# Kernel optimization log

Measured on AMD Instinct MI355X. Metric: run time of the kernel, lower is better.

Reference implementation:

```python
import jax, jax.numpy as jnp
import numpy as np

B, DIM, H, W = 2, 48, 256, 256
HEADS = 8
CHEAD = DIM // HEADS
HID = int(DIM * 2)


def _conv2d(x, w, stride=1, pad=0, dil=1, groups=1):
    return jax.lax.conv_general_dilated(
        x, w, (stride, stride), [(pad, pad), (pad, pad)],
        rhs_dilation=(dil, dil), feature_group_count=groups,
        dimension_numbers=('NCHW', 'OIHW', 'NCHW'))


def _ln(x, w, b):
    # WithBias LayerNorm over the channel axis (to_3d makes channels the last dim)
    mu = jnp.mean(x, axis=1, keepdims=True)
    var = jnp.mean((x - mu) ** 2, axis=1, keepdims=True)
    return (x - mu) / jnp.sqrt(var + 1e-5) * w[None, :, None, None] + b[None, :, None, None]


def _gelu(x):
    return jax.nn.gelu(x, approximate=False)


def setup_inputs() -> dict:
    key = jax.random.key(0)
    ks = iter(jax.random.split(key, 40))
    nrm = lambda *s: jax.random.normal(next(ks), s, dtype=jnp.float32) * 0.02
    d = dict(
        x=jax.random.normal(next(ks), (B, DIM, H, W), dtype=jnp.float32),
        ln1_w=jnp.ones(DIM), ln1_b=jnp.zeros(DIM),
        qkv_w=nrm(3 * DIM, DIM),            # 1x1x1 Conv3d == channel linear
        qkv_dw_w=nrm(3 * DIM, 1, 3, 3),     # center depth slice of 3x3x3 depthwise (depth=1 input)
        proj_w=nrm(DIM, DIM),
        fc_w=nrm(9, 3 * HEADS), fc_b=jnp.zeros(9),
        dep_w=nrm(DIM, 9, 3, 3), dep_b=jnp.zeros(DIM),  # groups = dim//heads
        l2q_w=nrm(DIM, DIM), l2q_b=jnp.zeros(DIM),
        temperature=jnp.ones(HEADS),
        ln2_w=jnp.ones(DIM), ln2_b=jnp.zeros(DIM),
        pin_w=nrm(3 * HID, DIM),
        dw1_w=nrm(HID, 1, 3, 3), dw2_w=nrm(HID, 1, 3, 3), dw3_w=nrm(HID, 1, 3, 3),
        pout_w=nrm(DIM, HID),
    )
    for i in range(3):
        d[f'cv_w{i}'] = nrm(DIM, DIM, 3, 3)
        d[f'cv_b{i}'] = jnp.zeros(DIM)
        d[f'cln_w{i}'] = jnp.ones(DIM)
        d[f'cln_b{i}'] = jnp.zeros(DIM)
    return d


def _forward(x, ln1_w, ln1_b, qkv_w, qkv_dw_w, proj_w, fc_w, fc_b, dep_w, dep_b,
             l2q_w, l2q_b, temperature, ln2_w, ln2_b, pin_w, dw1_w, dw2_w, dw3_w,
             pout_w, cv_w0, cv_b0, cln_w0, cln_b0, cv_w1, cv_b1, cln_w1, cln_b1,
             cv_w2, cv_b2, cln_w2, cln_b2):
    b, c, h, w = x.shape
    heads = temperature.shape[0]
    chead = c // heads

    # ---- Conv2DTransformer branch -> pooled descriptor x_d [b, c]
    t = x
    for cw, cb, lw, lb in ((cv_w0, cv_b0, cln_w0, cln_b0),
                           (cv_w1, cv_b1, cln_w1, cln_b1),
                           (cv_w2, cv_b2, cln_w2, cln_b2)):
        t = _conv2d(t, cw, stride=2, pad=1) + cb[None, :, None, None]
        t = jax.nn.relu(_ln(t, lw, lb))
        t = jax.lax.reduce_window(t, -jnp.inf, jax.lax.max, (1, 1, 2, 2), (1, 1, 2, 2), 'VALID')
    x_d = _gelu(jnp.mean(t, axis=(2, 3)))  # [b, c]

    # ---- Attention
    xn = _ln(x, ln1_w, ln1_b)
    qkv = jnp.einsum('oc,bchw->bohw', qkv_w, xn)
    qkv = _conv2d(qkv, qkv_dw_w, pad=1, groups=3 * c)  # depthwise, [b,3c,h,w]

    # conv-attention path: raw-memory reshape exactly as torch .reshape
    f_all = qkv.reshape(b, h * w, 3 * heads, chead).transpose(0, 2, 1, 3)  # [b,3H,hw,chead]
    f_all = jnp.einsum('oi,bipc->bopc', fc_w, f_all) + fc_b[None, :, None, None]  # [b,9,hw,chead]
    f_conv = f_all.transpose(0, 3, 1, 2).reshape(b, 9 * chead, h, w)
    out_conv = _conv2d(f_conv, dep_w, pad=1, groups=chead) + dep_b[None, :, None, None]

    # outer-product bias from pooled descriptor
    q0 = (x_d @ l2q_w.T + l2q_b).reshape(b, heads, chead)
    q0m = q0[:, :, :, None] * q0[:, :, None, :]  # [b,head,chead,chead]

    q, k, v = jnp.split(qkv, 3, axis=1)
    rs = lambda t_: t_.reshape(b, heads, chead, h * w)
    q, k, v = rs(q), rs(k), rs(v)
    nz = lambda t_: t_ / jnp.maximum(jnp.linalg.norm(t_, axis=-1, keepdims=True), 1e-12)
    q, k = nz(q), nz(k)

    attn = jnp.einsum('bhcx,bhdx->bhcd', q, k) * temperature[None, :, None, None]
    attn = jax.nn.softmax(attn * q0m, axis=-1)
    out = jnp.einsum('bhcd,bhdx->bhcx', attn, v).reshape(b, c, h, w)
    out = jnp.einsum('oc,bchw->bohw', proj_w, out) + out_conv

    x = x + out

    # ---- FeedForward (3-branch dilated depthwise)
    xn2 = _ln(x, ln2_w, ln2_b)
    y = jnp.einsum('oc,bchw->bohw', pin_w, xn2)  # [b,3*hid,h,w]
    hid = y.shape[1] // 3
    y1, y2, y3 = jnp.split(y, 3, axis=1)
    y1 = _conv2d(y1, dw1_w, pad=1, groups=hid)
    y2 = _conv2d(y2, dw2_w, pad=2, dil=2, groups=hid)
    y3 = _conv2d(y3, dw3_w, pad=3, dil=3, groups=hid)
    y = _gelu(y1) * y2 * y3
    return x + jnp.einsum('oc,bchw->bohw', pout_w, y)


def reference(x, ln1_w, ln1_b, qkv_w, qkv_dw_w, proj_w, fc_w, fc_b, dep_w, dep_b,
              l2q_w, l2q_b, temperature, ln2_w, ln2_b, pin_w, dw1_w, dw2_w, dw3_w,
              pout_w, cv_w0, cv_b0, cln_w0, cln_b0, cv_w1, cv_b1, cln_w1, cln_b1,
              cv_w2, cv_b2, cln_w2, cln_b2):
    return _forward(x, ln1_w, ln1_b, qkv_w, qkv_dw_w, proj_w, fc_w, fc_b, dep_w, dep_b,
                    l2q_w, l2q_b, temperature, ln2_w, ln2_b, pin_w, dw1_w, dw2_w, dw3_w,
                    pout_w, cv_w0, cv_b0, cln_w0, cln_b0, cv_w1, cv_b1, cln_w1, cln_b1,
                    cv_w2, cv_b2, cln_w2, cln_b2)
```

## Files before the change

### kernel.cpp

```cpp
#include <hip/hip_runtime.h>

constexpr int NB = 2;
constexpr int NC = 48;
constexpr int NH = 256;
constexpr int NW = 256;
constexpr int NP = NH * NW;
constexpr int NHEADS = 8;
constexpr int NCHD = 6;
constexpr int NHID = 96;
constexpr int GSEG = 64;

typedef unsigned short bf16_t;
typedef __attribute__((ext_vector_type(8))) short bf16x8;
typedef __attribute__((ext_vector_type(4))) float f32x4;

__device__ __forceinline__ float bf2f(bf16_t u) {
  union { unsigned int i; float f; } c; c.i = ((unsigned int)u) << 16; return c.f;
}
__device__ __forceinline__ bf16_t f2bf(float f) {
  union { float f; unsigned int i; } c; c.f = f;
  unsigned int r = (c.i + 0x7FFFu + ((c.i >> 16) & 1u)) >> 16;
  return (bf16_t)r;
}
__device__ __forceinline__ void unpack2(unsigned int u, float& a, float& b) {
  union { unsigned int i; float f; } c0, c1;
  c0.i = u << 16; c1.i = u & 0xffff0000u;
  a = c0.f; b = c1.f;
}

__device__ __forceinline__ float gelu_f(float v) {
  float u = v * (0.79788456f + 0.0356774081f * v * v);
  u = fminf(fmaxf(u, -9.f), 9.f);
  float e = __expf(-2.f * u);
  float th = (1.f - e) / (1.f + e);
  return 0.5f * v * (1.f + th);
}

#define STENCIL_ROW(LROW, D, WVAL0, WVAL1, WVAL2, ACC)                        \
  {                                                                            \
    const float* lp = &lds[(LROW) * 272 + quad * 4];                           \
    float4 va = *(const float4*)lp;                                            \
    float4 vb = *(const float4*)(lp + 4);                                      \
    float4 vc = *(const float4*)(lp + 8);                                      \
    float v[12] = {va.x, va.y, va.z, va.w, vb.x, vb.y, vb.z, vb.w,             \
                   vc.x, vc.y, vc.z, vc.w};                                    \
    _Pragma("unroll") for (int jj = 0; jj < 4; ++jj) {                         \
      ACC[jj] = fmaf(v[jj - (D) + 4], WVAL0, ACC[jj]);                         \
      ACC[jj] = fmaf(v[jj + 4], WVAL1, ACC[jj]);                               \
      ACC[jj] = fmaf(v[jj + (D) + 4], WVAL2, ACC[jj]);                         \
    }                                                                          \
  }

__global__ void k_prepw(const float* __restrict__ cvw0, bf16_t* __restrict__ WC) {
  int i = blockIdx.x * blockDim.x + threadIdx.x;
  if (i >= 9 * 3 * 2 * 512) return;
  int j = i & 7, lane = (i >> 3) & 63;
  int fi = i >> 9;
  int s = fi & 1;
  int tot = fi >> 1;
  int ot = tot % 3, t = tot / 3;
  int o = ot * 16 + (lane & 15);
  int k = s * 32 + ((lane >> 4) << 3) + j;
  float v = (k < 48) ? cvw0[(size_t)(o * 48 + k) * 9 + t] : 0.f;
  WC[i] = f2bf(v);
}

__global__ __launch_bounds__(512) void k_conv1_mfma(const float* __restrict__ in,
                                                    const bf16_t* __restrict__ WC,
                                                    const float* __restrict__ bias,
                                                    float* __restrict__ out) {
  __shared__ bf16_t xs[17 * 17 * 72];
  __shared__ float red[4 * 3 * 64 * 4];
  int blk = blockIdx.x;
  int tx = blk & 15;
  int t0 = blk >> 4;
  int ty = t0 & 15, b = t0 >> 4;
  int oy0 = ty * 8, ox0 = tx * 8;
  int iy0 = oy0 * 2 - 1, ix0 = ox0 * 2 - 1;
  const float* inb = in + (size_t)b * NC * NP;
  for (int i = threadIdx.x; i < 17 * 17 * 48; i += 512) {
    int cc = i % 17;
    int t2 = i / 17;
    int rr = t2 % 17;
    int ic = t2 / 17;
    float v = 0.f;
    int iy = iy0 + rr, ix = ix0 + cc;
    if ((unsigned)iy < 256u && (unsigned)ix < 256u)
      v = inb[((size_t)ic << 16) + (iy << 8) + ix];
    xs[(rr * 17 + cc) * 72 + ic] = f2bf(v);
  }
  for (int i = threadIdx.x; i < 289 * 16; i += 512) {
    int rcc = i >> 4, icz = i & 15;
    xs[rcc * 72 + 48 + icz] = 0;
  }
  __syncthreads();
  int wid = threadIdx.x >> 6, lane = threadIdx.x & 63;
  int pt = wid & 3, s = wid >> 2;
  int l15 = lane & 15, kl = lane >> 4;
  int px = pt * 16 + l15;
  int oy = px >> 3, ox = px & 7;
  int base = ((oy * 2) * 17 + ox * 2) * 72 + s * 32 + kl * 8;
  f32x4 acc[3] = {{0.f, 0.f, 0.f, 0.f}, {0.f, 0.f, 0.f, 0.f}, {0.f, 0.f, 0.f, 0.f}};
  #pragma unroll
  for (int t = 0; t < 9; ++t) {
    int dy = t / 3, dx = t % 3;
    bf16x8 bf = *(const bf16x8*)&xs[base + dy * (17 * 72) + dx * 72];
    #pragma unroll
    for (int ot = 0; ot < 3; ++ot) {
      bf16x8 af = *(const bf16x8*)(WC + (size_t)((t * 3 + ot) * 2 + s) * 512 + lane * 8);
      acc[ot] = __builtin_amdgcn_mfma_f32_16x16x32_bf16(af, bf, acc[ot], 0, 0, 0);
    }
  }
  if (s == 1) {
    #pragma unroll
    for (int ot = 0; ot < 3; ++ot)
      #pragma unroll
      for (int j = 0; j < 4; ++j)
        red[((pt * 3 + ot) * 64 + lane) * 4 + j] = acc[ot][j];
  }
  __syncthreads();
  if (s == 0) {
    float* ob = out + (size_t)b * NC * 16384;
    #pragma unroll
    for (int ot = 0; ot < 3; ++ot) {
      #pragma unroll
      for (int j = 0; j < 4; ++j) {
        int o = ot * 16 + kl * 4 + j;
        float r = acc[ot][j] + red[((pt * 3 + ot) * 64 + lane) * 4 + j] + bias[o];
        ob[((size_t)o * 128 + oy0 + oy) * 128 + ox0 + ox] = r;
      }
    }
  }
}

__global__ __launch_bounds__(512) void k_conv_s2_tile(const float* __restrict__ in,
                                                      const float* __restrict__ w,
                                                      const float* __restrict__ bias,
                                                      float* __restrict__ out,
                                                      int IH, int IW, int OH, int OW) {
  __shared__ float lds[16 * 442];
  int tilesX = OW >> 3;
  int tilesY = OH >> 3;
  int blk = blockIdx.x;
  int tx = blk % tilesX;
  int t = blk / tilesX;
  int ty = t % tilesY;
  int b = t / tilesY;
  int oy0 = ty * 8, ox0 = tx * 8;
  int iy0 = oy0 * 2 - 1, ix0 = ox0 * 2 - 1;
  const float* inb = in + (size_t)b * NC * IH * IW;

  int lane = threadIdx.x & 63;
  int oy = lane >> 3, ox = lane & 7;
  int ocb = __builtin_amdgcn_readfirstlane((threadIdx.x >> 6) * 6);
  float acc[6];
  #pragma unroll
  for (int j = 0; j < 6; ++j) acc[j] = bias[ocb + j];
  int rbase = oy * 52;

  for (int chunk = 0; chunk < 3; ++chunk) {
    int icb = chunk * 16;
    for (int i = threadIdx.x; i < 16 * 17 * 17; i += 512) {
      int cc = i % 17;
      int t2 = i / 17;
      int rr = t2 % 17;
      int ic = t2 / 17;
      float v = 0.f;
      int iy = iy0 + rr, ix = ix0 + cc;
      if ((unsigned)iy < (unsigned)IH && (unsigned)ix < (unsigned)IW)
        v = inb[((size_t)(icb + ic) * IH + iy) * IW + ix];
      lds[ic * 442 + rr * 26 + ((cc & 1) ? 13 + (cc >> 1) : (cc >> 1))] = v;
    }
    __syncthreads();

    for (int ic16 = 0; ic16 < 16; ++ic16) {
      const float* base = lds + ic16 * 442 + rbase;
      float e0[3], e1[3], ov[3];
      #pragma unroll
      for (int ky = 0; ky < 3; ++ky) {
        const float* rowp = base + ky * 26;
        e0[ky] = rowp[ox];
        e1[ky] = rowp[ox + 1];
        ov[ky] = rowp[13 + ox];
      }
      const float* wpc = w + (size_t)(ocb * 48 + icb + ic16) * 9;
      #pragma unroll
      for (int j = 0; j < 6; ++j) {
        const float* wp = wpc + (size_t)j * 48 * 9;
        float a = acc[j];
        #pragma unroll
        for (int ky = 0; ky < 3; ++ky) {
          a = fmaf(wp[ky * 3 + 0], e0[ky], a);
          a = fmaf(wp[ky * 3 + 1], ov[ky], a);
          a = fmaf(wp[ky * 3 + 2], e1[ky], a);
        }
        acc[j] = a;
      }
    }
    __syncthreads();
  }

  float* ob = out + (size_t)b * NC * OH * OW;
  #pragma unroll
  for (int j = 0; j < 6; ++j)
    ob[((size_t)(ocb + j) * OH + oy0 + oy) * OW + ox0 + ox] = acc[j];
}

__global__ void k_lnpool(const float* __restrict__ in, const float* __restrict__ lw,
                         const float* __restrict__ lb, float* __restrict__ out,
                         int IH, int IW) {
  int OH = IH >> 1, OW = IW >> 1;
  int idx = blockIdx.x * blockDim.x + threadIdx.x;
  int total = NB * OH * OW;
  if (idx >= total) return;
  int ox = idx % OW;
  int t = idx / OW;
  int oy = t % OH;
  int b = t / OH;
  const float* inb = in + (size_t)b * NC * IH * IW;
  float mu[4], rs[4];
  #pragma unroll
  for (int q = 0; q < 4; ++q) {
    int iy = oy * 2 + (q >> 1), ix = ox * 2 + (q & 1);
    float s = 0.f, ss = 0.f;
    for (int c = 0; c < NC; ++c) {
      float v = inb[((size_t)c * IH + iy) * IW + ix];
      s += v; ss += v * v;
    }
    float m = s * (1.f / NC);
    mu[q] = m;
    rs[q] = rsqrtf(fmaxf(ss * (1.f / NC) - m * m, 0.f) + 1e-5f);
  }
  for (int c = 0; c < NC; ++c) {
    float best = 0.f;
    float wv = lw[c], bv = lb[c];
    #pragma unroll
    for (int q = 0; q < 4; ++q) {
      int iy = oy * 2 + (q >> 1), ix = ox * 2 + (q & 1);
      float v = inb[((size_t)c * IH + iy) * IW + ix];
      v = (v - mu[q]) * rs[q] * wv + bv;
      best = fmaxf(best, fmaxf(v, 0.f));
    }
    out[((size_t)(b * NC + c) * OH + oy) * OW + ox] = best;
  }
}

__global__ void k_head(const float* __restrict__ p3, const float* __restrict__ l2qw,
                       const float* __restrict__ l2qb, float* __restrict__ q0m) {
  __shared__ float xd[NC], q0[NC];
  int b = blockIdx.x, t = threadIdx.x;
  if (t < NC) {
    float s = 0.f;
    for (int i = 0; i < 16; ++i) s += p3[(b * NC + t) * 16 + i];
    xd[t] = gelu_f(s * (1.f / 16.f));
  }
  __syncthreads();
  if (t < NC) {
    float a = l2qb[t];
    for (int c = 0; c < NC; ++c) a += xd[c] * l2qw[t * NC + c];
    q0[t] = a;
  }
  __syncthreads();
  if (t < NHEADS * NCHD * NCHD) {
    int h = t / 36, r = t % 36, c = r / 6, d = r % 6;
    q0m[b * 288 + t] = q0[h * 6 + c] * q0[h * 6 + d];
  }
}

__global__ void k_prep(const float* __restrict__ qkvw, const float* __restrict__ ln1w,
                       const float* __restrict__ ln1b, const float* __restrict__ pinw,
                       const float* __restrict__ ln2w, const float* __restrict__ ln2b,
                       const float* __restrict__ poutw, const float* __restrict__ projw,
                       float* __restrict__ SB, bf16_t* __restrict__ WA1,
                       bf16_t* __restrict__ WA2, bf16_t* __restrict__ WP,
                       bf16_t* __restrict__ WJ) {
  int t = blockIdx.x * blockDim.x + threadIdx.x;
  int stride = gridDim.x * blockDim.x;
  if (t < 144) {
    float s = 0.f, bb = 0.f;
    for (int c = 0; c < 48; ++c) {
      float w = qkvw[t * 48 + c];
      s = fmaf(w, ln1w[c], s); bb = fmaf(w, ln1b[c], bb);
    }
    SB[t] = s; SB[144 + t] = bb;
  } else if (t < 144 + 288) {
    int o = t - 144;
    float s = 0.f, bb = 0.f;
    for (int c = 0; c < 48; ++c) {
      float w = pinw[o * 48 + c];
      s = fmaf(w, ln2w[c], s); bb = fmaf(w, ln2b[c], bb);
    }
    SB[288 + o] = s; SB[576 + o] = bb;
  }
  for (int i = t; i < 9 * 1024; i += stride) {
    int j = i & 7, lane = (i >> 3) & 63, s = (i >> 9) & 1, ot = i >> 10;
    int o = ot * 16 + (lane & 15);
    int k = s * 32 + ((lane >> 4) << 3) + j;
    float v = (k < 48) ? qkvw[o * 48 + k] * ln1w[k] : 0.f;
    WA1[i] = f2bf(v);
  }
  for (int i = t; i < 18 * 1024; i += stride) {
    int j = i & 7, lane = (i >> 3) & 63, s = (i >> 9) & 1, ot = i >> 10;
    int o = ot * 16 + (lane & 15);
    int k = s * 32 + ((lane >> 4) << 3) + j;
    float v = (k < 48) ? pinw[o * 48 + k] * ln2w[k] : 0.f;
    WA2[i] = f2bf(v);
  }
  for (int i = t; i < 9 * 512; i += stride) {
    int j = i & 7, lane = (i >> 3) & 63;
    int fi = i >> 9;
    int s = fi % 3, ot = fi / 3;
    int o = ot * 16 + (lane & 15);
    int k = s * 32 + ((lane >> 4) << 3) + j;
    WP[i] = f2bf(poutw[o * 96 + k]);
  }
  for (int i = t; i < 6 * 512; i += stride) {
    int j = i & 7, lane = (i >> 3) & 63;
    int fi = i >> 9;
    int s = fi & 1, ot = fi >> 1;
    int o = ot * 16 + (lane & 15);
    int k = s * 32 + ((lane >> 4) << 3) + j;
    float v = (k < 48) ? projw[o * 48 + k] : 0.f;
    WJ[i] = f2bf(v);
  }
}

__global__ __launch_bounds__(256) void k_chmix_mfma(const float* __restrict__ x,
                                                    const bf16_t* __restrict__ WA,
                                                    const float* __restrict__ S,
                                                    const float* __restrict__ Bc,
                                                    bf16_t* __restrict__ out,
                                                    int nout) {
  __shared__ bf16_t xT[64 * 72];
  __shared__ float smu[64], srstd[64];
  int blk = blockIdx.x;
  int pxt = blk & 1023;
  int b = blk >> 10;
  int pbase = pxt * 64;
  const float* xb = x + (size_t)b * NC * NP + pbase;
  int p4 = threadIdx.x & 15, k0 = threadIdx.x >> 4;
  #pragma unroll
  for (int it = 0; it < 3; ++it) {
    int k = k0 + it * 16;
    float4 v = *(const float4*)(xb + (size_t)k * NP + p4 * 4);
    xT[(p4 * 4 + 0) * 72 + k] = f2bf(v.x);
    xT[(p4 * 4 + 1) * 72 + k] = f2bf(v.y);
    xT[(p4 * 4 + 2) * 72 + k] = f2bf(v.z);
    xT[(p4 * 4 + 3) * 72 + k] = f2bf(v.w);
  }
  {
    int k = 48 + k0;
    xT[(p4 * 4 + 0) * 72 + k] = 0;
    xT[(p4 * 4 + 1) * 72 + k] = 0;
    xT[(p4 * 4 + 2) * 72 + k] = 0;
    xT[(p4 * 4 + 3) * 72 + k] = 0;
  }
  __syncthreads();
  if (threadIdx.x < 64) {
    int t = threadIdx.x;
    float s = 0.f, ss = 0.f;
    #pragma unroll
    for (int k4 = 0; k4 < 12; ++k4) {
      ushort4 u = *(const ushort4*)&xT[t * 72 + k4 * 4];
      float a0 = bf2f(u.x), a1 = bf2f(u.y), a2 = bf2f(u.z), a3 = bf2f(u.w);
      s += a0 + a1 + a2 + a3;
      ss = fmaf(a0, a0, ss); ss = fmaf(a1, a1, ss);
      ss = fmaf(a2, a2, ss); ss = fmaf(a3, a3, ss);
    }
    float mu = s * (1.f / NC);
    smu[t] = mu;
    srstd[t] = rsqrtf(fmaxf(ss * (1.f / NC) - mu * mu, 0.f) + 1e-5f);
  }
  int w = threadIdx.x >> 6;
  int lane = threadIdx.x & 63;
  bf16x8 bfr0 = *(const bf16x8*)&xT[(w * 16 + (lane & 15)) * 72 + ((lane >> 4) << 3)];
  bf16x8 bfr1 = *(const bf16x8*)&xT[(w * 16 + (lane & 15)) * 72 + 32 + ((lane >> 4) << 3)];
  __syncthreads();
  float mu = smu[w * 16 + (lane & 15)];
  float rs = srstd[w * 16 + (lane & 15)];
  int p = pbase + w * 16 + (lane & 15);
  int nt = nout >> 4;
  bf16_t* ob = out + (size_t)b * nout * NP + p;
  for (int ot = 0; ot < nt; ++ot) {
    bf16x8 a0 = *(const bf16x8*)(WA + (size_t)(ot * 2 + 0) * 512 + lane * 8);
    bf16x8 a1 = *(const bf16x8*)(WA + (size_t)(ot * 2 + 1) * 512 + lane * 8);
    f32x4 acc = {0.f, 0.f, 0.f, 0.f};
    acc = __builtin_amdgcn_mfma_f32_16x16x32_bf16(a0, bfr0, acc, 0, 0, 0);
    acc = __builtin_amdgcn_mfma_f32_16x16x32_bf16(a1, bfr1, acc, 0, 0, 0);
    int orow = ot * 16 + ((lane >> 4) << 2);
    #pragma unroll
    for (int j = 0; j < 4; ++j) {
      int o = orow + j;
      float r = fmaf(rs, acc[j] - mu * S[o], Bc[o]);
      ob[(size_t)o * NP] = f2bf(r);
    }
  }
}

__global__ __launch_bounds__(256) void k_chmix_mfma_b(const bf16_t* __restrict__ x,
                                                      const bf16_t* __restrict__ WA,
                                                      const float* __restrict__ S,
                                                      const float* __restrict__ Bc,
                                                      bf16_t* __restrict__ out,
                                                      int nout) {
  __shared__ bf16_t xT[64 * 72];
  __shared__ float smu[64], srstd[64];
  int blk = blockIdx.x;
  int pxt = blk & 1023;
  int b = blk >> 10;
  int pbase = pxt * 64;
  const bf16_t* xb = x + (size_t)b * NC * NP + pbase;
  int p4 = threadIdx.x & 15, k0 = threadIdx.x >> 4;
  #pragma unroll
  for (int it = 0; it < 3; ++it) {
    int k = k0 + it * 16;
    ushort4 u = *(const ushort4*)(xb + (size_t)k * NP + p4 * 4);
    xT[(p4 * 4 + 0) * 72 + k] = u.x;
    xT[(p4 * 4 + 1) * 72 + k] = u.y;
    xT[(p4 * 4 + 2) * 72 + k] = u.z;
    xT[(p4 * 4 + 3) * 72 + k] = u.w;
  }
  {
    int k = 48 + k0;
    xT[(p4 * 4 + 0) * 72 + k] = 0;
    xT[(p4 * 4 + 1) * 72 + k] = 0;
    xT[(p4 * 4 + 2) * 72 + k] = 0;
    xT[(p4 * 4 + 3) * 72 + k] = 0;
  }
  __syncthreads();
  if (threadIdx.x < 64) {
    int t = threadIdx.x;
    float s = 0.f, ss = 0.f;
    #pragma unroll
    for (int k4 = 0; k4 < 12; ++k4) {
      ushort4 u = *(const ushort4*)&xT[t * 72 + k4 * 4];
      float a0 = bf2f(u.x), a1 = bf2f(u.y), a2 = bf2f(u.z), a3 = bf2f(u.w);
      s += a0 + a1 + a2 + a3;
      ss = fmaf(a0, a0, ss); ss = fmaf(a1, a1, ss);
      ss = fmaf(a2, a2, ss); ss = fmaf(a3, a3, ss);
    }
    float mu = s * (1.f / NC);
    smu[t] = mu;
    srstd[t] = rsqrtf(fmaxf(ss * (1.f / NC) - mu * mu, 0.f) + 1e-5f);
  }
  int w = threadIdx.x >> 6;
  int lane = threadIdx.x & 63;
  bf16x8 bfr0 = *(const bf16x8*)&xT[(w * 16 + (lane & 15)) * 72 + ((lane >> 4) << 3)];
  bf16x8 bfr1 = *(const bf16x8*)&xT[(w * 16 + (lane & 15)) * 72 + 32 + ((lane >> 4) << 3)];
  __syncthreads();
  float mu = smu[w * 16 + (lane & 15)];
  float rs = srstd[w * 16 + (lane & 15)];
  int p = pbase + w * 16 + (lane & 15);
  int nt = nout >> 4;
  bf16_t* ob = out + (size_t)b * nout * NP + p;
  for (int ot = 0; ot < nt; ++ot) {
    bf16x8 a0 = *(const bf16x8*)(WA + (size_t)(ot * 2 + 0) * 512 + lane * 8);
    bf16x8 a1 = *(const bf16x8*)(WA + (size_t)(ot * 2 + 1) * 512 + lane * 8);
    f32x4 acc = {0.f, 0.f, 0.f, 0.f};
    acc = __builtin_amdgcn_mfma_f32_16x16x32_bf16(a0, bfr0, acc, 0, 0, 0);
    acc = __builtin_amdgcn_mfma_f32_16x16x32_bf16(a1, bfr1, acc, 0, 0, 0);
    int orow = ot * 16 + ((lane >> 4) << 2);
    #pragma unroll
    for (int j = 0; j < 4; ++j) {
      int o = orow + j;
      float r = fmaf(rs, acc[j] - mu * S[o], Bc[o]);
      ob[(size_t)o * NP] = f2bf(r);
    }
  }
}

__global__ __launch_bounds__(256) void k_dw144(const bf16_t* __restrict__ in,
                                               const float* __restrict__ w9,
                                               bf16_t* __restrict__ out) {
  __shared__ float lds[6 * 272];
  int blk = blockIdx.x;
  int rq = blk & 63;
  int ch = (blk >> 6) % 144;
  int b = blk / (144 * 64);
  int yy0 = rq * 4;
  const bf16_t* ib = in + (size_t)(b * 144 + ch) * NP;
  for (int i = threadIdx.x; i < 6 * 68; i += 256) {
    int sr = i / 68, c4 = i % 68;
    int iy = yy0 + sr - 1;
    float4 v = make_float4(0.f, 0.f, 0.f, 0.f);
    if ((unsigned)iy < (unsigned)NH && c4 >= 1 && c4 <= 64) {
      ushort4 u = *(const ushort4*)(ib + iy * NW + (c4 - 1) * 4);
      v = make_float4(bf2f(u.x), bf2f(u.y), bf2f(u.z), bf2f(u.w));
    }
    *(float4*)(&lds[sr * 272 + c4 * 4]) = v;
  }
  __syncthreads();
  int q = threadIdx.x >> 6;
  int quad = threadIdx.x & 63;
  const float* wp = w9 + ch * 9;
  float acc[4] = {0.f, 0.f, 0.f, 0.f};
  #pragma unroll
  for (int rr = 0; rr < 3; ++rr)
    STENCIL_ROW(q + rr, 1, wp[rr * 3 + 0], wp[rr * 3 + 1], wp[rr * 3 + 2], acc);
  *(ushort4*)(out + (size_t)(b * 144 + ch) * NP + (yy0 + q) * NW + quad * 4) =
      make_ushort4(f2bf(acc[0]), f2bf(acc[1]), f2bf(acc[2]), f2bf(acc[3]));
}

__global__ __launch_bounds__(256) void k_gram(const bf16_t* __restrict__ qkvd,
                                              float* __restrict__ spart) {
  int gid = blockIdx.x;
  int seg = gid & (GSEG - 1), h = (gid >> 6) & 7, b = gid >> 9;
  const bf16_t* qb = qkvd + (size_t)(b * 144 + h * 6) * NP;
  const bf16_t* kb = qkvd + (size_t)(b * 144 + 48 + h * 6) * NP;
  float acc[48];
  #pragma unroll
  for (int j = 0; j < 48; ++j) acc[j] = 0.f;
  int p0 = seg * (NP / GSEG) + threadIdx.x * 4;
  float qv[6][4], kv[6][4];
  #pragma unroll
  for (int c = 0; c < 6; ++c) {
    ushort4 uq = *(const ushort4*)(qb + (size_t)c * NP + p0);
    qv[c][0] = bf2f(uq.x); qv[c][1] = bf2f(uq.y); qv[c][2] = bf2f(uq.z); qv[c][3] = bf2f(uq.w);
    ushort4 uk = *(const ushort4*)(kb + (size_t)c * NP + p0);
    kv[c][0] = bf2f(uk.x); kv[c][1] = bf2f(uk.y); kv[c][2] = bf2f(uk.z); kv[c][3] = bf2f(uk.w);
  }
  #pragma unroll
  for (int px = 0; px < 4; ++px) {
    #pragma unroll
    for (int c = 0; c < 6; ++c)
      #pragma unroll
      for (int d = 0; d < 6; ++d)
        acc[c * 6 + d] = fmaf(qv[c][px], kv[d][px], acc[c * 6 + d]);
    #pragma unroll
    for (int c = 0; c < 6; ++c) acc[36 + c] = fmaf(qv[c][px], qv[c][px], acc[36 + c]);
    #pragma unroll
    for (int d = 0; d < 6; ++d) acc[42 + d] = fmaf(kv[d][px], kv[d][px], acc[42 + d]);
  }
  int lane = threadIdx.x & 63, wid = threadIdx.x >> 6;
  __shared__ float sr[4 * 48];
  #pragma unroll
  for (int j = 0; j < 48; ++j) {
    float v = acc[j];
    #pragma unroll
    for (int off = 32; off; off >>= 1) v += __shfl_down(v, off, 64);
    if (lane == 0) sr[wid * 48 + j] = v;
  }
  __syncthreads();
  if (threadIdx.x < 48)
    spart[(size_t)gid * 48 + threadIdx.x] =
        sr[threadIdx.x] + sr[48 + threadIdx.x] + sr[96 + threadIdx.x] + sr[144 + threadIdx.x];
}

__global__ __launch_bounds__(256) void k_attn(const float* __restrict__ spart,
                                              const float* __restrict__ temp,
                                              const float* __restrict__ q0m,
                                              float* __restrict__ A) {
  int b = blockIdx.x;
  __shared__ float tot[8 * 48];
  for (int j = threadIdx.x; j < 384; j += 256) {
    int h = j / 48, v = j % 48;
    const float* base = spart + ((size_t)(b * 8 + h) * GSEG) * 48 + v;
    float s = 0.f;
    for (int seg = 0; seg < GSEG; ++seg) s += base[(size_t)seg * 48];
    tot[j] = s;
  }
  __syncthreads();
  int t = threadIdx.x;
  if (t >= 48) return;
  int h = t / 6, c = t % 6;
  const float* T = &tot[h * 48];
  float nq = fmaxf(sqrtf(T[36 + c]), 1e-12f);
  float tm = temp[h];
  float lg[6];
  #pragma unroll
  for (int d = 0; d < 6; ++d) {
    float nk = fmaxf(sqrtf(T[42 + d]), 1e-12f);
    lg[d] = (T[c * 6 + d] / (nq * nk)) * tm * q0m[b * 288 + h * 36 + c * 6 + d];
  }
  float m = lg[0];
  #pragma unroll
  for (int d = 1; d < 6; ++d) m = fmaxf(m, lg[d]);
  float sum = 0.f;
  #pragma unroll
  for (int d = 0; d < 6; ++d) { lg[d] = expf(lg[d] - m); sum += lg[d]; }
  float inv = 1.f / sum;
  #pragma unroll
  for (int d = 0; d < 6; ++d) A[b * 288 + h * 36 + c * 6 + d] = lg[d] * inv;
}

__global__ __launch_bounds__(384) void k_fc(const bf16_t* __restrict__ qkvd,
                                            const float* __restrict__ fcw,
                                            const float* __restrict__ fcb,
                                            bf16_t* __restrict__ fconv) {
  __shared__ float sin_[9216];
  __shared__ float sout[3456];
  int blk = blockIdx.x;
  int b = blk >> 10, p0 = (blk & 1023) << 6;
  const bf16_t* src = qkvd + (size_t)b * 144 * NP + (size_t)p0 * 144;
  const uint4* src4 = (const uint4*)src;
  for (int i = threadIdx.x; i < 1152; i += 384) {
    uint4 u = src4[i];
    float* d = &sin_[i * 8];
    unpack2(u.x, d[0], d[1]);
    unpack2(u.y, d[2], d[3]);
    unpack2(u.z, d[4], d[5]);
    unpack2(u.w, d[6], d[7]);
  }
  __syncthreads();
  int pl = threadIdx.x / 6, c2 = threadIdx.x % 6;
  float xv[24];
  #pragma unroll
  for (int g = 0; g < 24; ++g) xv[g] = sin_[pl * 144 + g * 6 + c2];
  #pragma unroll
  for (int o = 0; o < 9; ++o) {
    float a = fcb[o];
    #pragma unroll
    for (int g = 0; g < 24; ++g) a += fcw[o * 24 + g] * xv[g];
    sout[(c2 * 9 + o) * 64 + pl] = a;
  }
  __syncthreads();
  for (int i = threadIdx.x; i < 1728; i += 384) {
    int ch = i >> 5, pr = (i & 31) * 2;
    *(ushort2*)(fconv + (size_t)(b * 54 + ch) * NP + p0 + pr) =
        make_ushort2(f2bf(sout[ch * 64 + pr]), f2bf(sout[ch * 64 + pr + 1]));
  }
}

__global__ __launch_bounds__(256, 4) void k_depconv(const bf16_t* __restrict__ fconv,
                                                    const float* __restrict__ dw,
                                                    const float* __restrict__ db,
                                                    bf16_t* __restrict__ outconv) {
  __shared__ bf16_t lds16[9 * 6 * 272];
  int blk = blockIdx.x;
  int rq = blk & 63;
  int g = (blk >> 6) % 6;
  int b = blk / (6 * 64);
  int yy0 = rq * 4;
  const bf16_t* fb = fconv + (size_t)(b * 54 + g * 9) * NP;
  for (int i = threadIdx.x; i < 9 * 6 * 68; i += 256) {
    int j = i / 408;
    int rem = i % 408;
    int sr = rem / 68, c4 = rem % 68;
    int iy = yy0 + sr - 1;
    ushort4 v = make_ushort4(0, 0, 0, 0);
    if ((unsigned)iy < (unsigned)NH && c4 >= 1 && c4 <= 64)
      v = *(const ushort4*)(fb + (size_t)j * NP + iy * NW + (c4 - 1) * 4);
    *(ushort4*)(&lds16[(j * 6 + sr) * 272 + c4 * 4]) = v;
  }
  __syncthreads();
  int q = threadIdx.x >> 6;
  int quad = threadIdx.x & 63;
  float acc[8][4];
  #pragma unroll
  for (int o = 0; o < 8; ++o) {
    float bv = db[g * 8 + o];
    #pragma unroll
    for (int jj = 0; jj < 4; ++jj) acc[o][jj] = bv;
  }
  const float* wg = dw + (size_t)(g * 8) * 81;
  #pragma unroll
  for (int j = 0; j < 9; ++j) {
    #pragma unroll
    for (int rr = 0; rr < 3; ++rr) {
      const bf16_t* lp = &lds16[((j * 6) + q + rr) * 272 + quad * 4];
      ushort4 ua = *(const ushort4*)lp;
      ushort4 ub = *(const ushort4*)(lp + 4);
      ushort4 uc = *(const ushort4*)(lp + 8);
      float v[12] = {bf2f(ua.x), bf2f(ua.y), bf2f(ua.z), bf2f(ua.w),
                     bf2f(ub.x), bf2f(ub.y), bf2f(ub.z), bf2f(ub.w),
                     bf2f(uc.x), bf2f(uc.y), bf2f(uc.z), bf2f(uc.w)};
      #pragma unroll
      for (int dxi = 0; dxi < 3; ++dxi) {
        int wi = j * 9 + rr * 3 + dxi;
        #pragma unroll
        for (int o = 0; o < 8; ++o) {
          float wv = wg[o * 81 + wi];
          #pragma unroll
          for (int jj = 0; jj < 4; ++jj)
            acc[o][jj] = fmaf(v[jj + dxi + 3], wv, acc[o][jj]);
        }
      }
    }
  }
  bf16_t* ob = outconv + ((size_t)(b * NC + g * 8) * NH + yy0 + q) * NW + quad * 4;
  #pragma unroll
  for (int o = 0; o < 8; ++o)
    *(ushort4*)(ob + (size_t)o * NP) =
        make_ushort4(f2bf(acc[o][0]), f2bf(acc[o][1]), f2bf(acc[o][2]), f2bf(acc[o][3]));
}

__global__ __launch_bounds__(256) void k_proj_mfma(const bf16_t* __restrict__ qkvd,
                                                   const float* __restrict__ A,
                                                   const bf16_t* __restrict__ WJ,
                                                   const float* __restrict__ x,
                                                   const bf16_t* __restrict__ outconv,
                                                   bf16_t* __restrict__ x1) {
  __shared__ bf16_t vT[64 * 72];
  __shared__ bf16_t avT[64 * 72];
  __shared__ float sA[288];
  int blk = blockIdx.x;
  int pxt = blk & 1023;
  int b = blk >> 10;
  int pbase = pxt * 64;
  const bf16_t* vb = qkvd + (size_t)(b * 144 + 96) * NP + pbase;
  int p4 = threadIdx.x & 15, k0 = threadIdx.x >> 4;
  #pragma unroll
  for (int it = 0; it < 3; ++it) {
    int k = k0 + it * 16;
    ushort4 u = *(const ushort4*)(vb + (size_t)k * NP + p4 * 4);
    vT[(p4 * 4 + 0) * 72 + k] = u.x;
    vT[(p4 * 4 + 1) * 72 + k] = u.y;
    vT[(p4 * 4 + 2) * 72 + k] = u.z;
    vT[(p4 * 4 + 3) * 72 + k] = u.w;
  }
  {
    int k = 48 + k0;
    avT[(p4 * 4 + 0) * 72 + k] = 0;
    avT[(p4 * 4 + 1) * 72 + k] = 0;
    avT[(p4 * 4 + 2) * 72 + k] = 0;
    avT[(p4 * 4 + 3) * 72 + k] = 0;
  }
  for (int i = threadIdx.x; i < 288; i += 256) sA[i] = A[b * 288 + i];
  __syncthreads();
  {
    int px = threadIdx.x & 63, hh = threadIdx.x >> 6;
    #pragma unroll
    for (int hi = 0; hi < 2; ++hi) {
      int h = hh * 2 + hi;
      float v6[6];
      #pragma unroll
      for (int d = 0; d < 6; ++d) v6[d] = bf2f(vT[px * 72 + h * 6 + d]);
      #pragma unroll
      for (int c = 0; c < 6; ++c) {
        float av = 0.f;
        #pragma unroll
        for (int d = 0; d < 6; ++d) av = fmaf(sA[h * 36 + c * 6 + d], v6[d], av);
        avT[px * 72 + h * 6 + c] = f2bf(av);
      }
    }
  }
  __syncthreads();
  int w = threadIdx.x >> 6;
  int lane = threadIdx.x & 63;
  int prow = w * 16 + (lane & 15);
  bf16x8 f0 = *(const bf16x8*)&avT[prow * 72 + ((lane >> 4) << 3)];
  bf16x8 f1 = *(const bf16x8*)&avT[prow * 72 + 32 + ((lane >> 4) << 3)];
  int p = pbase + prow;
  const float* xb = x + (size_t)b * NC * NP + p;
  const bf16_t* ob = outconv + (size_t)b * NC * NP + p;
  bf16_t* x1b = x1 + (size_t)b * NC * NP + p;
  #pragma unroll
  for (int ot = 0; ot < 3; ++ot) {
    bf16x8 a0 = *(const bf16x8*)(WJ + (size_t)(ot * 2 + 0) * 512 + lane * 8);
    bf16x8 a1 = *(const bf16x8*)(WJ + (size_t)(ot * 2 + 1) * 512 + lane * 8);
    f32x4 acc = {0.f, 0.f, 0.f, 0.f};
    acc = __builtin_amdgcn_mfma_f32_16x16x32_bf16(a0, f0, acc, 0, 0, 0);
    acc = __builtin_amdgcn_mfma_f32_16x16x32_bf16(a1, f1, acc, 0, 0, 0);
    int orow = ot * 16 + ((lane >> 4) << 2);
    #pragma unroll
    for (int j = 0; j < 4; ++j) {
      int o = orow + j;
      x1b[(size_t)o * NP] = f2bf(xb[(size_t)o * NP] + acc[j] + bf2f(ob[(size_t)o * NP]));
    }
  }
}

__global__ __launch_bounds__(256) void k_ffdw(const bf16_t* __restrict__ y,
                                              const float* __restrict__ w1,
                                              const float* __restrict__ w2,
                                              const float* __restrict__ w3,
                                              bf16_t* __restrict__ z) {
  __shared__ float lds[24 * 272];
  int blk = blockIdx.x;
  int rq = blk & 63;
  int ch = (blk >> 6) % NHID;
  int b = blk / (NHID * 64);
  int yy0 = rq * 4;
  const bf16_t* yb = y + (size_t)(b * 288 + ch) * NP;
  if (threadIdx.x < 96) {
    int sr = threadIdx.x >> 2, part = threadIdx.x & 3;
    int slot = (part == 0) ? 0 : (256 + part * 4);
    *(float4*)(&lds[sr * 272 + slot]) = make_float4(0.f, 0.f, 0.f, 0.f);
  }
  #pragma unroll
  for (int it = 0; it < 6; ++it) {
    int sr = (threadIdx.x >> 6) + it * 4;
    int m = threadIdx.x & 63;
    int br, iy;
    if (sr < 6)       { br = 0; iy = yy0 + sr - 1; }
    else if (sr < 14) { br = 1; iy = yy0 + sr - 8; }
    else              { br = 2; iy = yy0 + sr - 17; }
    float4 v = make_float4(0.f, 0.f, 0.f, 0.f);
    if ((unsigned)iy < (unsigned)NH) {
      ushort4 u = *(const ushort4*)(yb + (size_t)(br * NHID) * NP + iy * NW + m * 4);
      v = make_float4(bf2f(u.x), bf2f(u.y), bf2f(u.z), bf2f(u.w));
    }
    *(float4*)(&lds[sr * 272 + 4 + m * 4]) = v;
  }
  __syncthreads();
  int q = threadIdx.x >> 6;
  int quad = threadIdx.x & 63;
  const float* wp1 = w1 + ch * 9;
  const float* wp2 = w2 + ch * 9;
  const float* wp3 = w3 + ch * 9;
  float c1[4] = {0.f, 0.f, 0.f, 0.f};
  float c2[4] = {0.f, 0.f, 0.f, 0.f};
  float c3[4] = {0.f, 0.f, 0.f, 0.f};
  #pragma unroll
  for (int rr = 0; rr < 3; ++rr)
    STENCIL_ROW(0 + q + rr * 1, 1, wp1[rr * 3 + 0], wp1[rr * 3 + 1], wp1[rr * 3 + 2], c1);
  #pragma unroll
  for (int rr = 0; rr < 3; ++rr)
    STENCIL_ROW(6 + q + rr * 2, 2, wp2[rr * 3 + 0], wp2[rr * 3 + 1], wp2[rr * 3 + 2], c2);
  #pragma unroll
  for (int rr = 0; rr < 3; ++rr)
    STENCIL_ROW(14 + q + rr * 3, 3, wp3[rr * 3 + 0], wp3[rr * 3 + 1], wp3[rr * 3 + 2], c3);
  *(ushort4*)(z + (size_t)(b * NHID + ch) * NP + (yy0 + q) * NW + quad * 4) =
      make_ushort4(f2bf(gelu_f(c1[0]) * c2[0] * c3[0]),
                   f2bf(gelu_f(c1[1]) * c2[1] * c3[1]),
                   f2bf(gelu_f(c1[2]) * c2[2] * c3[2]),
                   f2bf(gelu_f(c1[3]) * c2[3] * c3[3]));
}

__global__ __launch_bounds__(256) void k_pout_mfma(const bf16_t* __restrict__ z,
                                                   const bf16_t* __restrict__ WP,
                                                   const bf16_t* __restrict__ x1,
                                                   float* __restrict__ outp) {
  __shared__ bf16_t zT[64 * 104];
  int blk = blockIdx.x;
  int pxt = blk & 1023;
  int b = blk >> 10;
  int pbase = pxt * 64;
  const bf16_t* zb = z + (size_t)b * NHID * NP + pbase;
  int p4 = threadIdx.x & 15, k0 = threadIdx.x >> 4;
  #pragma unroll
  for (int it = 0; it < 6; ++it) {
    int k = k0 + it * 16;
    ushort4 u = *(const ushort4*)(zb + (size_t)k * NP + p4 * 4);
    zT[(p4 * 4 + 0) * 104 + k] = u.x;
    zT[(p4 * 4 + 1) * 104 + k] = u.y;
    zT[(p4 * 4 + 2) * 104 + k] = u.z;
    zT[(p4 * 4 + 3) * 104 + k] = u.w;
  }
  __syncthreads();
  int w = threadIdx.x >> 6;
  int lane = threadIdx.x & 63;
  int prow = w * 16 + (lane & 15);
  bf16x8 bfr[3];
  #pragma unroll
  for (int s = 0; s < 3; ++s)
    bfr[s] = *(const bf16x8*)&zT[prow * 104 + s * 32 + ((lane >> 4) << 3)];
  int p = pbase + prow;
  const bf16_t* x1b = x1 + (size_t)b * NC * NP + p;
  float* ob = outp + (size_t)b * NC * NP + p;
  #pragma unroll
  for (int ot = 0; ot < 3; ++ot) {
    f32x4 acc = {0.f, 0.f, 0.f, 0.f};
    #pragma unroll
    for (int s = 0; s < 3; ++s) {
      bf16x8 a = *(const bf16x8*)(WP + (size_t)(ot * 3 + s) * 512 + lane * 8);
      acc = __builtin_amdgcn_mfma_f32_16x16x32_bf16(a, bfr[s], acc, 0, 0, 0);
    }
    int orow = ot * 16 + ((lane >> 4) << 2);
    #pragma unroll
    for (int j = 0; j < 4; ++j) {
      int o = orow + j;
      ob[(size_t)o * NP] = bf2f(x1b[(size_t)o * NP]) + acc[j];
    }
  }
}

constexpr size_t SZ_QKV = (size_t)NB * 144 * NP;
constexpr size_t SZ_CHW = (size_t)NB * NC * NP;
constexpr size_t OFF_QKV0 = 0;
constexpr size_t OFF_QKVD = OFF_QKV0 + SZ_QKV;
constexpr size_t OFF_FCONV = OFF_QKVD + SZ_QKV;
constexpr size_t SZ_FCONV = (size_t)NB * 54 * NP;
constexpr size_t OFF_OUTCONV = OFF_FCONV + SZ_FCONV;
constexpr size_t OFF_X1 = OFF_OUTCONV + SZ_CHW;
constexpr size_t OFF_STATS = OFF_X1 + SZ_CHW;
constexpr size_t OFF_T1 = OFF_STATS + (size_t)NB * NP * 2;
constexpr size_t OFF_P1 = OFF_T1 + (size_t)NB * NC * 128 * 128;
constexpr size_t OFF_T2 = OFF_P1 + (size_t)NB * NC * 64 * 64;
constexpr size_t OFF_P2 = OFF_T2 + (size_t)NB * NC * 32 * 32;
constexpr size_t OFF_T3 = OFF_P2 + (size_t)NB * NC * 16 * 16;
constexpr size_t OFF_P3 = OFF_T3 + (size_t)NB * NC * 8 * 8;
constexpr size_t OFF_Q0M = OFF_P3 + (size_t)NB * NC * 4 * 4;
constexpr size_t OFF_NORMS = OFF_Q0M + 576;
constexpr size_t OFF_SPART = OFF_NORMS + 192;
constexpr size_t OFF_A = OFF_SPART + (size_t)NB * 64 * 48;

extern "C" void kernel_launch(void* const* d_in, const int* in_sizes, int n_in,
                              void* d_out, int out_size, void* d_ws, size_t ws_size,
                              hipStream_t stream) {
  const float* x     = (const float*)d_in[0];
  const float* ln1w  = (const float*)d_in[1];
  const float* ln1b  = (const float*)d_in[2];
  const float* qkvw  = (const float*)d_in[3];
  const float* qkvdw = (const float*)d_in[4];
  const float* projw = (const float*)d_in[5];
  const float* fcw   = (const float*)d_in[6];
  const float* fcb   = (const float*)d_in[7];
  const float* depw  = (const float*)d_in[8];
  const float* depb  = (const float*)d_in[9];
  const float* l2qw  = (const float*)d_in[10];
  const float* l2qb  = (const float*)d_in[11];
  const float* temp  = (const float*)d_in[12];
  const float* ln2w  = (const float*)d_in[13];
  const float* ln2b  = (const float*)d_in[14];
  const float* pinw  = (const float*)d_in[15];
  const float* dw1   = (const float*)d_in[16];
  const float* dw2   = (const float*)d_in[17];
  const float* dw3   = (const float*)d_in[18];
  const float* poutw = (const float*)d_in[19];
  const float* cvw0  = (const float*)d_in[20];
  const float* cvb0  = (const float*)d_in[21];
  const float* clw0  = (const float*)d_in[22];
  const float* clb0  = (const float*)d_in[23];
  const float* cvw1  = (const float*)d_in[24];
  const float* cvb1  = (const float*)d_in[25];
  const float* clw1  = (const float*)d_in[26];
  const float* clb1  = (const float*)d_in[27];
  const float* cvw2  = (const float*)d_in[28];
  const float* cvb2  = (const float*)d_in[29];
  const float* clw2  = (const float*)d_in[30];
  const float* clb2  = (const float*)d_in[31];

  float* ws = (float*)d_ws;
  bf16_t* qkv0 = (bf16_t*)(ws + OFF_QKV0);
  bf16_t* qkvd = (bf16_t*)(ws + OFF_QKVD);
  bf16_t* fconv = (bf16_t*)(ws + OFF_FCONV);
  bf16_t* outconv = (bf16_t*)(ws + OFF_OUTCONV);
  bf16_t* x1 = (bf16_t*)(ws + OFF_X1);
  float* t1 = ws + OFF_T1;
  float* p1 = ws + OFF_P1;
  float* t2 = ws + OFF_T2;
  float* p2 = ws + OFF_P2;
  float* t3 = ws + OFF_T3;
  float* p3 = ws + OFF_P3;
  float* q0m = ws + OFF_Q0M;
  float* spart = ws + OFF_STATS;
  float* A = ws + OFF_SPART;
  float* SB = ws + OFF_T1;
  bf16_t* WA1 = (bf16_t*)(ws + OFF_T1 + 1024);
  bf16_t* WA2 = (bf16_t*)(ws + OFF_T1 + 1024 + 4608);
  bf16_t* WP  = (bf16_t*)(ws + OFF_T1 + 1024 + 4608 + 9216);
  bf16_t* WJ  = (bf16_t*)(ws + OFF_T1 + 1024 + 4608 + 9216 + 2304);
  bf16_t* WC = (bf16_t*)(ws + OFF_QKV0);
  bf16_t* ybuf = (bf16_t*)(ws + OFF_QKV0);
  bf16_t* zbuf = (bf16_t*)(ws + OFF_FCONV);

  k_prepw<<<108, 256, 0, stream>>>(cvw0, WC);
  k_conv1_mfma<<<512, 512, 0, stream>>>(x, WC, cvb0, t1);
  k_lnpool<<<32, 256, 0, stream>>>(t1, clw0, clb0, p1, 128, 128);
  k_conv_s2_tile<<<32, 512, 0, stream>>>(p1, cvw1, cvb1, t2, 64, 64, 32, 32);
  k_lnpool<<<2, 256, 0, stream>>>(t2, clw1, clb1, p2, 32, 32);
  k_conv_s2_tile<<<2, 512, 0, stream>>>(p2, cvw2, cvb2, t3, 16, 16, 8, 8);
  k_lnpool<<<1, 256, 0, stream>>>(t3, clw2, clb2, p3, 8, 8);
  k_head<<<2, 320, 0, stream>>>(p3, l2qw, l2qb, q0m);

  k_prep<<<8, 256, 0, stream>>>(qkvw, ln1w, ln1b, pinw, ln2w, ln2b, poutw, projw,
                                SB, WA1, WA2, WP, WJ);

  k_chmix_mfma<<<NB * 1024, 256, 0, stream>>>(x, WA1, SB, SB + 144, qkv0, 144);
  k_dw144<<<NB * 144 * 64, 256, 0, stream>>>(qkv0, qkvdw, qkvd);
  k_gram<<<NB * NHEADS * GSEG, 256, 0, stream>>>(qkvd, spart);
  k_attn<<<2, 256, 0, stream>>>(spart, temp, q0m, A);
  k_fc<<<2048, 384, 0, stream>>>(qkvd, fcw, fcb, fconv);
  k_depconv<<<768, 256, 0, stream>>>(fconv, depw, depb, outconv);
  k_proj_mfma<<<NB * 1024, 256, 0, stream>>>(qkvd, A, WJ, x, outconv, x1);

  k_chmix_mfma_b<<<NB * 1024, 256, 0, stream>>>(x1, WA2, SB + 288, SB + 576, ybuf, 288);
  k_ffdw<<<NB * NHID * 64, 256, 0, stream>>>(ybuf, dw1, dw2, dw3, zbuf);
  k_pout_mfma<<<NB * 1024, 256, 0, stream>>>(zbuf, WP, x1, (float*)d_out);
}
```

Baseline: 365.2 us.

## Enlarge depthwise row tile and pad LDS strides in fc kernel

```diff
diff --git a/kernel.cpp b/kernel.cpp
--- a/kernel.cpp
+++ b/kernel.cpp
@@ -472,33 +472,43 @@
 __global__ __launch_bounds__(256) void k_dw144(const bf16_t* __restrict__ in,
                                                const float* __restrict__ w9,
                                                bf16_t* __restrict__ out) {
-  __shared__ float lds[6 * 272];
+  __shared__ float lds[10 * 272];
   int blk = blockIdx.x;
-  int rq = blk & 63;
-  int ch = (blk >> 6) % 144;
-  int b = blk / (144 * 64);
-  int yy0 = rq * 4;
+  int rq = blk & 31;
+  int ch = (blk >> 5) % 144;
+  int b = blk / (144 * 32);
+  int yy0 = rq * 8;
   const bf16_t* ib = in + (size_t)(b * 144 + ch) * NP;
-  for (int i = threadIdx.x; i < 6 * 68; i += 256) {
-    int sr = i / 68, c4 = i % 68;
+  if (threadIdx.x < 40) {
+    int sr = threadIdx.x >> 2, part = threadIdx.x & 3;
+    int slot = (part == 0) ? 0 : (256 + part * 4);
+    *(float4*)(&lds[sr * 272 + slot]) = make_float4(0.f, 0.f, 0.f, 0.f);
+  }
+  for (int i = threadIdx.x; i < 640; i += 256) {
+    int sr = i >> 6, m = i & 63;
     int iy = yy0 + sr - 1;
     float4 v = make_float4(0.f, 0.f, 0.f, 0.f);
-    if ((unsigned)iy < (unsigned)NH && c4 >= 1 && c4 <= 64) {
-      ushort4 u = *(const ushort4*)(ib + iy * NW + (c4 - 1) * 4);
+    if ((unsigned)iy < (unsigned)NH) {
+      ushort4 u = *(const ushort4*)(ib + iy * NW + m * 4);
       v = make_float4(bf2f(u.x), bf2f(u.y), bf2f(u.z), bf2f(u.w));
     }
-    *(float4*)(&lds[sr * 272 + c4 * 4]) = v;
+    *(float4*)(&lds[sr * 272 + 4 + m * 4]) = v;
   }
   __syncthreads();
   int q = threadIdx.x >> 6;
   int quad = threadIdx.x & 63;
   const float* wp = w9 + ch * 9;
-  float acc[4] = {0.f, 0.f, 0.f, 0.f};
-  #pragma unroll
-  for (int rr = 0; rr < 3; ++rr)
-    STENCIL_ROW(q + rr, 1, wp[rr * 3 + 0], wp[rr * 3 + 1], wp[rr * 3 + 2], acc);
-  *(ushort4*)(out + (size_t)(b * 144 + ch) * NP + (yy0 + q) * NW + quad * 4) =
-      make_ushort4(f2bf(acc[0]), f2bf(acc[1]), f2bf(acc[2]), f2bf(acc[3]));
+  bf16_t* ob = out + (size_t)(b * 144 + ch) * NP;
+  #pragma unroll
+  for (int half = 0; half < 2; ++half) {
+    int orow = q + half * 4;
+    float acc[4] = {0.f, 0.f, 0.f, 0.f};
+    #pragma unroll
+    for (int rr = 0; rr < 3; ++rr)
+      STENCIL_ROW(orow + rr, 1, wp[rr * 3 + 0], wp[rr * 3 + 1], wp[rr * 3 + 2], acc);
+    *(ushort4*)(ob + (yy0 + orow) * NW + quad * 4) =
+        make_ushort4(f2bf(acc[0]), f2bf(acc[1]), f2bf(acc[2]), f2bf(acc[3]));
+  }
 }
 
 __global__ __launch_bounds__(256) void k_gram(const bf16_t* __restrict__ qkvd,
@@ -587,15 +597,16 @@
                                             const float* __restrict__ fcw,
                                             const float* __restrict__ fcb,
                                             bf16_t* __restrict__ fconv) {
-  __shared__ float sin_[9216];
-  __shared__ float sout[3456];
+  __shared__ float sin_[64 * 148];
+  __shared__ float sout[54 * 66];
   int blk = blockIdx.x;
   int b = blk >> 10, p0 = (blk & 1023) << 6;
   const bf16_t* src = qkvd + (size_t)b * 144 * NP + (size_t)p0 * 144;
   const uint4* src4 = (const uint4*)src;
   for (int i = threadIdx.x; i < 1152; i += 384) {
     uint4 u = src4[i];
-    float* d = &sin_[i * 8];
+    int pix = i / 18, sub = i % 18;
+    float* d = &sin_[pix * 148 + sub * 8];
     unpack2(u.x, d[0], d[1]);
     unpack2(u.y, d[2], d[3]);
     unpack2(u.z, d[4], d[5]);
@@ -605,19 +616,19 @@
   int pl = threadIdx.x / 6, c2 = threadIdx.x % 6;
   float xv[24];
   #pragma unroll
-  for (int g = 0; g < 24; ++g) xv[g] = sin_[pl * 144 + g * 6 + c2];
+  for (int g = 0; g < 24; ++g) xv[g] = sin_[pl * 148 + g * 6 + c2];
   #pragma unroll
   for (int o = 0; o < 9; ++o) {
     float a = fcb[o];
     #pragma unroll
     for (int g = 0; g < 24; ++g) a += fcw[o * 24 + g] * xv[g];
-    sout[(c2 * 9 + o) * 64 + pl] = a;
+    sout[(c2 * 9 + o) * 66 + pl] = a;
   }
   __syncthreads();
   for (int i = threadIdx.x; i < 1728; i += 384) {
     int ch = i >> 5, pr = (i & 31) * 2;
     *(ushort2*)(fconv + (size_t)(b * 54 + ch) * NP + p0 + pr) =
-        make_ushort2(f2bf(sout[ch * 64 + pr]), f2bf(sout[ch * 64 + pr + 1]));
+        make_ushort2(f2bf(sout[ch * 66 + pr]), f2bf(sout[ch * 66 + pr + 1]));
   }
 }
 
@@ -958,7 +969,7 @@
                                 SB, WA1, WA2, WP, WJ);
 
   k_chmix_mfma<<<NB * 1024, 256, 0, stream>>>(x, WA1, SB, SB + 144, qkv0, 144);
-  k_dw144<<<NB * 144 * 64, 256, 0, stream>>>(qkv0, qkvdw, qkvd);
+  k_dw144<<<NB * 144 * 32, 256, 0, stream>>>(qkv0, qkvdw, qkvd);
   k_gram<<<NB * NHEADS * GSEG, 256, 0, stream>>>(qkvd, spart);
   k_attn<<<2, 256, 0, stream>>>(spart, temp, q0m, A);
   k_fc<<<2048, 384, 0, stream>>>(qkvd, fcw, fcb, fconv);
```

Result: no change. 363.4 us (-0.5%).
